# Kernel optimization log

Measured on AMD Instinct MI355X. Metric: run time of the kernel, lower is better.

The kernel has to match this reference:

```python
import jax, jax.numpy as jnp
import numpy as np

N, L, H, E, FE = 32, 128, 16, 256, 4  # batch, seq_len, heads, embed_size, forward_expansion
EPS = 1e-5
NEG_SLOPE = 0.01


def _mask_positions(qe):
    # zero entries where j < L-1-i (torch: triu(ones,1).flip(1) == 1)
    Ld = qe.shape[-1]
    i = jnp.arange(Ld)[:, None]
    j = jnp.arange(Ld)[None, :]
    return jnp.where(j >= (Ld - 1 - i), qe, jnp.zeros((), qe.dtype))


def _skew(qe):
    # pad last dim on the left, reinterpret, drop first row -> relative skew
    n, h, Ld, _ = qe.shape
    p = jnp.pad(qe, ((0, 0), (0, 0), (0, 0), (1, 0)))
    return p.reshape(n, h, Ld + 1, Ld)[:, :, 1:, :]


def _batchnorm(x, gamma, beta):
    # BatchNorm1d(C=L*H) over (N, C, E): normalize over batch and embed dims
    mean = jnp.mean(x, axis=(0, 2), keepdims=True)
    var = jnp.var(x, axis=(0, 2), keepdims=True)
    return (x - mean) * jax.lax.rsqrt(var + EPS) * gamma[None, :, None] + beta[None, :, None]


def _leaky(x):
    return jnp.where(x >= 0, x, NEG_SLOPE * x)


def setup_inputs() -> dict:
    key = jax.random.key(0)
    ks = jax.random.split(key, 16)
    s_e = 1.0 / np.sqrt(E)
    d = {
        "x": jax.random.normal(ks[0], (N, L * H, E, 1), dtype=jnp.float32),
        "Wq": jax.random.normal(ks[1], (E, E), dtype=jnp.float32) * s_e,
        "bq": jnp.zeros((E,), jnp.float32),
        "Wk": jax.random.normal(ks[2], (E, E), dtype=jnp.float32) * s_e,
        "bk": jnp.zeros((E,), jnp.float32),
        "Wv": jax.random.normal(ks[3], (E, E), dtype=jnp.float32) * s_e,
        "bv": jnp.zeros((E,), jnp.float32),
        "Erel": jax.random.normal(ks[4], (H, L, E), dtype=jnp.float32),
        "Wo": jax.random.normal(ks[5], (E, E), dtype=jnp.float32) * s_e,
        "bo": jnp.zeros((E,), jnp.float32),
        "g1": jnp.ones((L * H,), jnp.float32),
        "be1": jnp.zeros((L * H,), jnp.float32),
        "g2": jnp.ones((L * H,), jnp.float32),
        "be2": jnp.zeros((L * H,), jnp.float32),
        "W1": jax.random.normal(ks[6], (E, FE * E), dtype=jnp.float32) * s_e,
        "b1": jnp.zeros((FE * E,), jnp.float32),
        "W2": jax.random.normal(ks[7], (FE * E, E), dtype=jnp.float32) * (1.0 / np.sqrt(FE * E)),
        "b2": jnp.zeros((E,), jnp.float32),
        "Wenc": jax.random.normal(ks[8], (E, E), dtype=jnp.float32) * s_e,
        "benc": jnp.zeros((E,), jnp.float32),
    }
    return d


def reference(x, Wq, bq, Wk, bk, Wv, bv, Erel, Wo, bo, g1, be1, g2, be2, W1, b1, W2, b2, Wenc, benc):
    xs = x[:, :, :, 0]  # (N, L*H, E)
    q = (xs @ Wq + bq).reshape(N, L, H, E)
    k = (xs @ Wk + bk).reshape(N, L, H, E)
    v = (xs @ Wv + bv).reshape(N, L, H, E)
    # relative-position skew term (Music-Transformer style)
    QE = jnp.einsum('nlhe,hme->nhlm', q, Erel)       # (N,H,L,L)
    S = _skew(_mask_positions(QE))                   # (N,H,L,L)
    qk = jnp.einsum('nqhe,nkhe->nhqk', q, k)         # (N,H,L,L)
    att = jax.nn.softmax(qk / jnp.sqrt(jnp.float32(E)), axis=-1) + S
    z = jnp.einsum('nhql,nlhe->nqhe', att, v).reshape(N, L * H, E)
    z = z @ Wo + bo
    h1 = _batchnorm(z + xs, g1, be1)
    ff = _leaky(h1 @ W1 + b1) @ W2 + b2
    out = _batchnorm(ff + h1, g2, be2)
    return out @ Wenc + benc
```

## Files before the change

### kernel.cpp

```cpp
#include <hip/hip_runtime.h>
#include <hip/hip_bf16.h>

using u16 = unsigned short;
typedef __attribute__((ext_vector_type(8))) short bf16x8;
typedef __attribute__((ext_vector_type(4))) float f32x4;

static constexpr float EPS_ = 1e-5f;
static constexpr float NEG_ = 0.01f;

__device__ __forceinline__ float bf2f(u16 u) { return __uint_as_float(((unsigned)u) << 16); }
__device__ __forceinline__ u16 f2bf(float f) {
    union { __hip_bfloat16 h; u16 u; } c; c.h = __float2bfloat16(f); return c.u;
}

#define MFMA16(a, b, c) __builtin_amdgcn_mfma_f32_16x16x32_bf16(a, b, c, 0, 0, 0)

__device__ __forceinline__ void gload16(const u16* g, u16* l) {
    __builtin_amdgcn_global_load_lds(
        (__attribute__((address_space(1))) void*)(u16*)g,
        (__attribute__((address_space(3))) void*)l, 16, 0, 0);
}

__device__ __forceinline__ int xswz(int nwg) {
    const int b = blockIdx.x;
    return (b & 7) * (nwg >> 3) + (b >> 3);
}

__device__ __forceinline__ void lds_core(
    const u16* __restrict__ Ag, int lda,
    const u16* __restrict__ Bg, int ldb, int K,
    u16* As, u16* Bs, f32x4 acc[4][4])
{
    const int tid = threadIdx.x;
    const int w = tid >> 6, lane = tid & 63;
    const int g = lane >> 4, r = lane & 15;
    const int wm = (w >> 1) * 64, wn = (w & 1) * 64;
    const int rx = r & 7;

    for (int kt = 0; kt < K; kt += 64) {
        #pragma unroll
        for (int j = 0; j < 4; j++) {
            const int ubase = (w * 4 + j) * 64;
            const int u = ubase + lane;
            const int row = u >> 3;
            const int cb = ((u & 7) ^ (row & 7)) * 8;
            gload16(Ag + (size_t)row * lda + kt + cb, As + ubase * 8);
            gload16(Bg + (size_t)row * ldb + kt + cb, Bs + ubase * 8);
        }
        __syncthreads();
        #pragma unroll
        for (int kk = 0; kk < 2; kk++) {
            const int co = ((kk * 4 + g) ^ rx) * 8;
            bf16x8 af[4], bfr[4];
            #pragma unroll
            for (int f = 0; f < 4; f++) {
                af[f]  = *(const bf16x8*)(As + (wm + f * 16 + r) * 64 + co);
                bfr[f] = *(const bf16x8*)(Bs + (wn + f * 16 + r) * 64 + co);
            }
            #pragma unroll
            for (int i = 0; i < 4; i++)
                #pragma unroll
                for (int j = 0; j < 4; j++)
                    acc[i][j] = MFMA16(af[i], bfr[j], acc[i][j]);
        }
        __syncthreads();
    }
}

__device__ __forceinline__ void zero4(f32x4 acc[4][4]) {
    #pragma unroll
    for (int i = 0; i < 4; i++)
        #pragma unroll
        for (int j = 0; j < 4; j++)
            acc[i][j] = (f32x4){0.f, 0.f, 0.f, 0.f};
}

template<int K, int NN, int MODE>
__global__ __launch_bounds__(256) void gemm128_k(
    const u16* __restrict__ A, const u16* __restrict__ Bt,
    const float* __restrict__ bias, const u16* __restrict__ res,
    const float2* __restrict__ rp, const float* __restrict__ cs,
    void* __restrict__ outv)
{
    __shared__ __align__(16) u16 SH[17408];
    u16* As = SH; u16* Bs = SH + 8192;
    constexpr int NB = NN / 128;
    const int f = xswz(512 * NB);
    const int m0 = (f / NB) * 128, n0 = (f % NB) * 128;

    f32x4 acc[4][4]; zero4(acc);
    lds_core(A + (size_t)m0 * K, K, Bt + (size_t)n0 * K, K, K, As, Bs, acc);

    const int tid = threadIdx.x;
    const int w = tid >> 6, lane = tid & 63;
    const int g = lane >> 4, r = lane & 15;
    const int mb = (w >> 1) * 64, nb = (w & 1) * 64;

    __syncthreads();

    if constexpr (MODE == 3) {
        float* SHf = (float*)SH;
        float* out = (float*)outv;
        #pragma unroll
        for (int q = 0; q < 4; ++q) {
            if ((w >> 1) == (q >> 1)) {
                const int fmB = (q & 1) * 2;
                #pragma unroll
                for (int fi = 0; fi < 2; ++fi) {
                    #pragma unroll
                    for (int fn = 0; fn < 4; ++fn) {
                        const int col = nb + fn * 16 + r;
                        const float bv = bias[n0 + col], cv = cs[n0 + col];
                        #pragma unroll
                        for (int reg = 0; reg < 4; ++reg) {
                            const int rl = fi * 16 + g * 4 + reg;
                            const int m = m0 + q * 32 + rl;
                            const float2 pp = rp[m & 2047];
                            SHf[rl * 132 + col] =
                                pp.x * acc[fmB + fi][fn][reg] + pp.y * cv + bv;
                        }
                    }
                }
            }
            __syncthreads();
            #pragma unroll
            for (int p = 0; p < 4; ++p) {
                const int id = p * 256 + tid;
                const int rl = id >> 5, c4 = id & 31;
                const float4 v = *(const float4*)(SHf + rl * 132 + c4 * 4);
                *(float4*)(out + (size_t)(m0 + q * 32 + rl) * 256 + n0 + c4 * 4) = v;
            }
            __syncthreads();
        }
        return;
    }

    u16* out = (u16*)outv;
    #pragma unroll
    for (int fn = 0; fn < 4; ++fn) {
        const int col = nb + fn * 16 + r;
        const float bv = bias[n0 + col];
        #pragma unroll
        for (int fm = 0; fm < 4; ++fm) {
            #pragma unroll
            for (int reg = 0; reg < 4; ++reg) {
                const int rowt = mb + fm * 16 + g * 4 + reg;
                float v = acc[fm][fn][reg];
                if constexpr (MODE == 1) {
                    const float2 pp = rp[(m0 + rowt) & 2047];
                    v = pp.x * v + pp.y * cs[n0 + col] + bv;
                    v = v >= 0.f ? v : NEG_ * v;
                } else {
                    v += bv;
                }
                SH[rowt * 136 + col] = f2bf(v);
            }
        }
    }
    __syncthreads();
    #pragma unroll
    for (int p = 0; p < 8; ++p) {
        const int ck = p * 256 + tid;
        const int rowt = ck >> 4, cc = ck & 15;
        const int m = m0 + rowt;
        bf16x8 v = *(const bf16x8*)(SH + rowt * 136 + cc * 8);
        if constexpr (MODE == 0) {
            const bf16x8 rv = *(const bf16x8*)(res + (size_t)m * NN + n0 + cc * 8);
            #pragma unroll
            for (int j = 0; j < 8; ++j)
                v[j] = (short)f2bf(bf2f((u16)v[j]) + bf2f((u16)rv[j]));
        }
        if constexpr (MODE == 2) {
            const float2 pp = rp[m & 2047];
            const bf16x8 rv = *(const bf16x8*)(res + (size_t)m * NN + n0 + cc * 8);
            #pragma unroll
            for (int j = 0; j < 8; ++j)
                v[j] = (short)f2bf(bf2f((u16)v[j]) + pp.x * bf2f((u16)rv[j]) + pp.y);
        }
        *(bf16x8*)(out + (size_t)m * NN + n0 + cc * 8) = v;
    }
}

__global__ __launch_bounds__(256) void qkv_k(
    const u16* __restrict__ xbf, const u16* __restrict__ Wqkvt,
    const float* __restrict__ bq, const float* __restrict__ bk,
    const float* __restrict__ bv,
    u16* __restrict__ qo, u16* __restrict__ ko, u16* __restrict__ vo)
{
    __shared__ __align__(16) u16 SH[17408];
    u16* As = SH; u16* Bs = SH + 8192;
    const int f = xswz(3072);
    const int nblk = f % 6, mblk = f / 6;
    const int m0 = mblk * 128, n0 = nblk * 128;
    const int which = n0 >> 8;
    const float* bias = which == 0 ? bq : (which == 1 ? bk : bv);
    const int e0 = n0 & 255;

    f32x4 acc[4][4]; zero4(acc);
    lds_core(xbf + (size_t)m0 * 256, 256, Wqkvt + (size_t)n0 * 256, 256, 256,
             As, Bs, acc);

    const int tid = threadIdx.x;
    const int w = tid >> 6, lane = tid & 63;
    const int g = lane >> 4, r = lane & 15;
    const int mb = (w >> 1) * 64, nb = (w & 1) * 64;
    const int nn = m0 >> 11, l0 = (m0 & 2047) >> 4;

    __syncthreads();
    if (which == 2) {
        #pragma unroll
        for (int fn = 0; fn < 4; ++fn) {
            const int col = nb + fn * 16 + r;
            const float bv4 = bias[e0 + col];
            #pragma unroll
            for (int fm = 0; fm < 4; ++fm)
                #pragma unroll
                for (int reg = 0; reg < 4; ++reg) {
                    const int rowt = mb + fm * 16 + g * 4 + reg;
                    SH[col * 136 + (((rowt & 15) << 3) | (rowt >> 4))] =
                        f2bf(acc[fm][fn][reg] + bv4);
                }
        }
        __syncthreads();
        #pragma unroll
        for (int p = 0; p < 8; ++p) {
            const int ck = p * 256 + tid;
            const int e = ck >> 4, hh = ck & 15;
            const bf16x8 v = *(const bf16x8*)(SH + e * 136 + hh * 8);
            *(bf16x8*)(vo + ((size_t)(nn * 16 + hh) * 256 + e0 + e) * 128 + l0) = v;
        }
    } else {
        u16* out = which == 0 ? qo : ko;
        #pragma unroll
        for (int fn = 0; fn < 4; ++fn) {
            const int col = nb + fn * 16 + r;
            const float bv4 = bias[e0 + col];
            #pragma unroll
            for (int fm = 0; fm < 4; ++fm)
                #pragma unroll
                for (int reg = 0; reg < 4; ++reg) {
                    const int rowt = mb + fm * 16 + g * 4 + reg;
                    SH[rowt * 136 + col] = f2bf(acc[fm][fn][reg] + bv4);
                }
        }
        __syncthreads();
        #pragma unroll
        for (int p = 0; p < 8; ++p) {
            const int ck = p * 256 + tid;
            const int rowt = ck >> 4, cc = ck & 15;
            const int m = m0 + rowt;
            const int l = (m & 2047) >> 4, hh = m & 15;
            const bf16x8 v = *(const bf16x8*)(SH + rowt * 136 + cc * 8);
            *(bf16x8*)(out + ((size_t)(nn * 16 + hh) * 128 + l) * 256 + e0 + cc * 8) = v;
        }
    }
}

template<typename OutF>
__device__ __forceinline__ void epi_store128(
    u16* Cs, f32x4 (&acc)[4][4], float scale, OutF outp)
{
    const int tid = threadIdx.x;
    const int w = tid >> 6, lane = tid & 63;
    const int g = lane >> 4, r = lane & 15;
    const int mb = (w >> 1) * 64, nb = (w & 1) * 64;

    #pragma unroll
    for (int fn = 0; fn < 4; fn++) {
        const int col = nb + fn * 16 + r;
        #pragma unroll
        for (int fm = 0; fm < 4; fm++)
            #pragma unroll
            for (int reg = 0; reg < 4; reg++) {
                const int row = mb + fm * 16 + g * 4 + reg;
                Cs[row * 136 + col] = f2bf(acc[fm][fn][reg] * scale);
            }
    }
    __syncthreads();
    #pragma unroll
    for (int p = 0; p < 8; p++) {
        const int ck = p * 256 + tid;
        const int row = ck >> 4, cc = ck & 15;
        const bf16x8 v = *(const bf16x8*)(Cs + row * 136 + cc * 8);
        *(bf16x8*)outp(row, cc) = v;
    }
}

__global__ __launch_bounds__(256) void qkqe_k(
    const u16* __restrict__ q, const u16* __restrict__ kc,
    const u16* __restrict__ erel, u16* __restrict__ out)
{
    __shared__ __align__(16) u16 SH[17408];
    u16* As = SH; u16* Bs = SH + 8192;
    const int f = xswz(1024);
    const int b = f >> 1, h = b & 15;
    const int n0 = (f & 1) * 128;
    const u16* Ag = q + (size_t)b * 128 * 256;
    const u16* Bg = (n0 == 0) ? (kc + (size_t)b * 128 * 256)
                              : (erel + (size_t)h * 128 * 256);

    f32x4 acc[4][4]; zero4(acc);
    lds_core(Ag, 256, Bg, 256, 256, As, Bs, acc);

    const float scale = (n0 == 0) ? 0.0625f : 1.0f;
    __syncthreads();
    epi_store128(SH, acc, scale,
        [&](int row, int cc) -> u16* {
            return out + ((size_t)b * 128 + row) * 256 + n0 + cc * 8;
        });
}

__global__ __launch_bounds__(256) void softmax_k(
    const u16* __restrict__ qk, u16* __restrict__ att)
{
    const int r = blockIdx.x * 4 + (threadIdx.x >> 6);
    const int lane = threadIdx.x & 63;
    const int i = r & 127;
    const u16* row = qk + (size_t)r * 256;
    const float x0 = bf2f(row[lane]), x1 = bf2f(row[lane + 64]);
    float mx = fmaxf(x0, x1);
    #pragma unroll
    for (int o = 32; o; o >>= 1) mx = fmaxf(mx, __shfl_xor(mx, o));
    const float e0 = __expf(x0 - mx), e1 = __expf(x1 - mx);
    float s = e0 + e1;
    #pragma unroll
    for (int o = 32; o; o >>= 1) s += __shfl_xor(s, o);
    const float rinv = 1.0f / s;
    const float s0 = (lane <= i) ? bf2f(row[128 + 127 - i + lane]) : 0.f;
    const float s1 = (lane + 64 <= i) ? bf2f(row[128 + 127 - i + lane + 64]) : 0.f;
    att[(size_t)r * 128 + lane] = f2bf(e0 * rinv + s0);
    att[(size_t)r * 128 + lane + 64] = f2bf(e1 * rinv + s1);
}

__global__ __launch_bounds__(256) void av_k(
    const u16* __restrict__ att, const u16* __restrict__ vT,
    u16* __restrict__ zc)
{
    __shared__ __align__(16) u16 SH[17408];
    u16* As = SH; u16* Bs = SH + 8192;
    const int f = xswz(1024);
    const int b = f >> 1;
    const int n0 = (f & 1) * 128;
    const u16* Ag = att + (size_t)b * 128 * 128;
    const u16* Bg = vT + (size_t)b * 256 * 128 + (size_t)n0 * 128;

    f32x4 acc[4][4]; zero4(acc);
    lds_core(Ag, 128, Bg, 128, 128, As, Bs, acc);

    const int nn = b >> 4, hh = b & 15;
    __syncthreads();
    epi_store128(SH, acc, 1.f,
        [&](int row, int cc) -> u16* {
            return zc + ((size_t)(nn * 2048 + row * 16 + hh)) * 256 + n0 + cc * 8;
        });
}

__global__ __launch_bounds__(256) void cvt_k(const float* __restrict__ in,
                                             u16* __restrict__ out) {
    const size_t i8 = ((size_t)blockIdx.x * 256 + threadIdx.x) * 8;
    const float4 lo = *(const float4*)(in + i8);
    const float4 hi = *(const float4*)(in + i8 + 4);
    ushort4 o0, o1;
    o0.x = f2bf(lo.x); o0.y = f2bf(lo.y); o0.z = f2bf(lo.z); o0.w = f2bf(lo.w);
    o1.x = f2bf(hi.x); o1.y = f2bf(hi.y); o1.z = f2bf(hi.z); o1.w = f2bf(hi.w);
    *(ushort4*)(out + i8) = o0;
    *(ushort4*)(out + i8 + 4) = o1;
}

__global__ __launch_bounds__(256) void prep_w_k(
    const float* __restrict__ Wq, const float* __restrict__ Wk,
    const float* __restrict__ Wv, const float* __restrict__ Wo,
    const float* __restrict__ Wenc, const float* __restrict__ W1,
    const float* __restrict__ W2, const float* __restrict__ Erel,
    u16* __restrict__ Wqkvt, u16* __restrict__ Wot, u16* __restrict__ Wenct,
    u16* __restrict__ W1t, u16* __restrict__ W2t, u16* __restrict__ Erelb,
    float* __restrict__ cs1, float* __restrict__ csE)
{
    const int bid = blockIdx.x, tid = threadIdx.x;
    if (bid < 1280) {
        const int jb = bid >> 8;
        const int t = ((bid & 255) << 8) | tid;
        const int n = t >> 8, k = t & 255;
        const float* src = jb == 0 ? Wq : jb == 1 ? Wk : jb == 2 ? Wv
                         : jb == 3 ? Wo : Wenc;
        const u16 v = f2bf(src[(k << 8) + n]);
        if (jb < 3)       Wqkvt[jb * 65536 + t] = v;
        else if (jb == 3) Wot[t] = v;
        else              Wenct[t] = v;
    } else if (bid < 2304) {
        const int t = ((bid - 1280) << 8) | tid;
        const int n = t >> 8, k = t & 255;
        W1t[t] = f2bf(W1[(k << 10) + n]);
    } else if (bid < 3328) {
        const int t = ((bid - 2304) << 8) | tid;
        const int n = t >> 10, k = t & 1023;
        W2t[t] = f2bf(W2[(k << 8) + n]);
    } else if (bid < 5376) {
        const int t = ((bid - 3328) << 8) | tid;
        Erelb[t] = f2bf(Erel[t]);
    } else {
        const int n = (bid - 5376) * 256 + tid;
        if (n < 1024) {
            float s = 0.f;
            for (int k = 0; k < 256; ++k) s += bf2f(f2bf(W1[(size_t)k * 1024 + n]));
            cs1[n] = s;
        } else {
            const int n2 = n - 1024;
            float s = 0.f;
            for (int k = 0; k < 256; ++k) s += bf2f(f2bf(Wenc[(size_t)k * 256 + n2]));
            csE[n2] = s;
        }
    }
}

__global__ __launch_bounds__(256) void bnstats_k(
    const u16* __restrict__ x, const float* __restrict__ g,
    const float* __restrict__ be, float2* __restrict__ params)
{
    const int c = blockIdx.x, tid = threadIdx.x;
    float s = 0.f, s2 = 0.f;
    #pragma unroll 4
    for (int n = 0; n < 32; n++) {
        const float v = bf2f(x[((size_t)n * 2048 + c) * 256 + tid]);
        s += v; s2 += v * v;
    }
    #pragma unroll
    for (int o = 32; o; o >>= 1) { s += __shfl_xor(s, o); s2 += __shfl_xor(s2, o); }
    __shared__ float rs[4], rs2[4];
    const int w = tid >> 6;
    if ((tid & 63) == 0) { rs[w] = s; rs2[w] = s2; }
    __syncthreads();
    if (tid == 0) {
        s  = rs[0] + rs[1] + rs[2] + rs[3];
        s2 = rs2[0] + rs2[1] + rs2[2] + rs2[3];
        const float mean = s / 8192.f;
        const float var = s2 / 8192.f - mean * mean;
        const float a = g[c] * rsqrtf(var + EPS_);
        params[c] = make_float2(a, be[c] - mean * a);
    }
}

extern "C" void kernel_launch(void* const* d_in, const int* in_sizes, int n_in,
                              void* d_out, int out_size, void* d_ws, size_t ws_size,
                              hipStream_t stream)
{
    const float* x    = (const float*)d_in[0];
    const float* Wq   = (const float*)d_in[1];
    const float* bq   = (const float*)d_in[2];
    const float* Wk   = (const float*)d_in[3];
    const float* bk   = (const float*)d_in[4];
    const float* Wv   = (const float*)d_in[5];
    const float* bv   = (const float*)d_in[6];
    const float* Erel = (const float*)d_in[7];
    const float* Wo   = (const float*)d_in[8];
    const float* bo   = (const float*)d_in[9];
    const float* g1   = (const float*)d_in[10];
    const float* be1  = (const float*)d_in[11];
    const float* g2   = (const float*)d_in[12];
    const float* be2  = (const float*)d_in[13];
    const float* W1   = (const float*)d_in[14];
    const float* b1   = (const float*)d_in[15];
    const float* W2   = (const float*)d_in[16];
    const float* b2   = (const float*)d_in[17];
    const float* Wenc = (const float*)d_in[18];
    const float* benc = (const float*)d_in[19];

    char* ws = (char*)d_ws;
    const size_t MB = 1ull << 20;
    const size_t KB = 1024;
    u16* xbf   = (u16*)(ws + 0 * MB);
    u16* h2pre = (u16*)(ws + 32 * MB);
    u16* qb    = (u16*)(ws + 32 * MB);
    u16* kb    = (u16*)(ws + 64 * MB);
    u16* vT    = (u16*)(ws + 96 * MB);
    u16* qkb   = (u16*)(ws + 128 * MB);
    u16* attb  = (u16*)(ws + 160 * MB);
    u16* ff1   = (u16*)(ws + 64 * MB);
    u16* zc    = (u16*)(ws + 176 * MB);
    u16* h1pre = (u16*)(ws + 208 * MB);
    u16* Wqkvt = (u16*)(ws + 240 * MB);
    u16* Wot   = (u16*)(ws + 240 * MB + 512 * KB);
    u16* Wenct = (u16*)(ws + 240 * MB + 640 * KB);
    u16* W1t   = (u16*)(ws + 240 * MB + 768 * KB);
    u16* W2t   = (u16*)(ws + 240 * MB + 1280 * KB);
    u16* Erelb = (u16*)(ws + 240 * MB + 1792 * KB);
    float2* p1 = (float2*)(ws + 243 * MB);
    float2* p2 = (float2*)(ws + 243 * MB + 16 * KB);
    float* cs1 = (float*)(ws + 243 * MB + 32 * KB);
    float* csE = (float*)(ws + 243 * MB + 40 * KB);

    const dim3 b256(256);

    cvt_k<<<dim3(8192), b256, 0, stream>>>(x, xbf);
    prep_w_k<<<dim3(5381), b256, 0, stream>>>(Wq, Wk, Wv, Wo, Wenc, W1, W2, Erel,
                                              Wqkvt, Wot, Wenct, W1t, W2t, Erelb,
                                              cs1, csE);

    qkv_k<<<dim3(3072), b256, 0, stream>>>(xbf, Wqkvt, bq, bk, bv, qb, kb, vT);
    qkqe_k<<<dim3(1024), b256, 0, stream>>>(qb, kb, Erelb, qkb);
    softmax_k<<<dim3(16384), b256, 0, stream>>>(qkb, attb);
    av_k<<<dim3(1024), b256, 0, stream>>>(attb, vT, zc);
    gemm128_k<256, 256, 0><<<dim3(1024), b256, 0, stream>>>(
        zc, Wot, bo, xbf, nullptr, nullptr, h1pre);

    bnstats_k<<<dim3(2048), b256, 0, stream>>>(h1pre, g1, be1, p1);

    gemm128_k<256, 1024, 1><<<dim3(4096), b256, 0, stream>>>(
        h1pre, W1t, b1, nullptr, p1, cs1, ff1);
    gemm128_k<1024, 256, 2><<<dim3(1024), b256, 0, stream>>>(
        ff1, W2t, b2, h1pre, p1, nullptr, h2pre);

    bnstats_k<<<dim3(2048), b256, 0, stream>>>(h2pre, g2, be2, p2);
    gemm128_k<256, 256, 3><<<dim3(1024), b256, 0, stream>>>(
        h2pre, Wenct, benc, nullptr, p2, csE, (float*)d_out);
}
```

Measured before the change: 330.9 us.

## Use persistent B-panel-resident GEMMs with triple-buffered A staging for K=256 projections

```diff
diff --git a/kernel.cpp b/kernel.cpp
--- a/kernel.cpp
+++ b/kernel.cpp
@@ -24,6 +24,270 @@
 __device__ __forceinline__ int xswz(int nwg) {
     const int b = blockIdx.x;
     return (b & 7) * (nwg >> 3) + (b >> 3);
+}
+
+__device__ __forceinline__ void zero4(f32x4 acc[4][4]) {
+    #pragma unroll
+    for (int i = 0; i < 4; i++)
+        #pragma unroll
+        for (int j = 0; j < 4; j++)
+            acc[i][j] = (f32x4){0.f, 0.f, 0.f, 0.f};
+}
+
+__device__ __forceinline__ void bp_stageA(const u16* __restrict__ A,
+                                          int mrow_base, int ki, u16* dst) {
+    const int tid = threadIdx.x;
+    #pragma unroll
+    for (int j = 0; j < 4; ++j) {
+        const int u = j * 256 + tid;
+        const int row = u >> 3, slot = u & 7;
+        gload16(A + (size_t)(mrow_base + row) * 256 + ki * 64 +
+                    ((slot ^ (row & 7)) * 8),
+                dst + u * 8);
+    }
+}
+
+template<int MT, class EPIF>
+__device__ __forceinline__ void bp_run(
+    const u16* __restrict__ A, int m0base,
+    const u16* __restrict__ Btp,
+    u16* SH, EPIF epi)
+{
+    const int tid = threadIdx.x;
+    const int w = tid >> 6, lane = tid & 63;
+    const int g = lane >> 4, r = lane & 15;
+    const int wm = (w >> 1) * 64, wn = (w & 1) * 64;
+    const int rx = r & 7;
+    u16* Bp = SH;
+    u16* Ab0 = SH + 32768; u16* Ab1 = SH + 40960; u16* Ab2 = SH + 49152;
+    u16* Ab[3] = {Ab0, Ab1, Ab2};
+
+    #pragma unroll
+    for (int it = 0; it < 16; ++it) {
+        const int u = it * 256 + tid;
+        const int col = u >> 5, slot = u & 31;
+        gload16(Btp + (size_t)col * 256 + ((slot ^ (col & 7)) * 8), Bp + u * 8);
+    }
+    bp_stageA(A, m0base, 0, Ab[0]);
+    bp_stageA(A, m0base, 1, Ab[1]);
+
+    int cur = 0;
+    for (int mi = 0; mi < MT; ++mi) {
+        f32x4 acc[4][4]; zero4(acc);
+        const int mrow = m0base + mi * 128;
+        #pragma unroll
+        for (int ki = 0; ki < 4; ++ki) {
+            if (!(mi > 0 && ki == 0)) {
+                if (mi == MT - 1 && ki == 3)
+                    asm volatile("s_waitcnt vmcnt(0)" ::: "memory");
+                else
+                    asm volatile("s_waitcnt vmcnt(4)" ::: "memory");
+                __builtin_amdgcn_s_barrier();
+                __builtin_amdgcn_sched_barrier(0);
+            }
+            const u16* Abuf = Ab[cur];
+            const int nb = cur + 2 >= 3 ? cur - 1 : cur + 2;
+            if (ki == 0)      bp_stageA(A, mrow, 2, Ab[nb]);
+            else if (ki == 1) bp_stageA(A, mrow, 3, Ab[nb]);
+            else if (ki == 2) { if (mi + 1 < MT) bp_stageA(A, mrow + 128, 0, Ab[nb]); }
+            else              { if (mi + 1 < MT) bp_stageA(A, mrow + 128, 1, Ab[nb]); }
+            #pragma unroll
+            for (int kk = 0; kk < 2; ++kk) {
+                const int co = ((kk * 4 + g) ^ rx) * 8;
+                bf16x8 af[4], bfr[4];
+                #pragma unroll
+                for (int f2 = 0; f2 < 4; ++f2) {
+                    af[f2]  = *(const bf16x8*)(Abuf + (wm + f2 * 16 + r) * 64 + co);
+                    bfr[f2] = *(const bf16x8*)(Bp +
+                                (size_t)(wn + f2 * 16 + r) * 256 + ki * 64 + co);
+                }
+                __builtin_amdgcn_s_setprio(1);
+                #pragma unroll
+                for (int i = 0; i < 4; i++)
+                    #pragma unroll
+                    for (int j = 0; j < 4; j++)
+                        acc[i][j] = MFMA16(af[i], bfr[j], acc[i][j]);
+                __builtin_amdgcn_s_setprio(0);
+            }
+            cur = cur + 1 == 3 ? 0 : cur + 1;
+        }
+        epi(mrow, acc);
+        asm volatile("s_waitcnt vmcnt(0)" ::: "memory");
+        __builtin_amdgcn_s_barrier();
+        __builtin_amdgcn_sched_barrier(0);
+    }
+}
+
+template<int NPAN, int MT, int MODE, int NN>
+__global__ __launch_bounds__(256) void gemmBP_k(
+    const u16* __restrict__ A, const u16* __restrict__ Bt,
+    const float* __restrict__ bias, const u16* __restrict__ res,
+    const float2* __restrict__ rp, const float* __restrict__ cs,
+    void* __restrict__ outv)
+{
+    __shared__ __align__(16) u16 SH[74752];
+    const int f = xswz(NPAN * (512 / MT));
+    const int panel = f % NPAN, mg = f / NPAN;
+    const int n0 = panel * 128;
+    const int m0base = mg * MT * 128;
+    u16* EPIB = SH + 57344;
+
+    const int tid = threadIdx.x;
+    const int w = tid >> 6, lane = tid & 63;
+    const int g = lane >> 4, r = lane & 15;
+    const int mb = (w >> 1) * 64, nb = (w & 1) * 64;
+
+    auto epi = [&](int mrow, f32x4 (&acc)[4][4]) {
+        if constexpr (MODE == 3) {
+            float* SHf = (float*)EPIB;
+            float* out = (float*)outv;
+            #pragma unroll
+            for (int q = 0; q < 4; ++q) {
+                if ((w >> 1) == (q >> 1)) {
+                    const int fmB = (q & 1) * 2;
+                    #pragma unroll
+                    for (int fi = 0; fi < 2; ++fi)
+                        #pragma unroll
+                        for (int fn = 0; fn < 4; ++fn) {
+                            const int col = nb + fn * 16 + r;
+                            const float bv = bias[n0 + col], cv = cs[n0 + col];
+                            #pragma unroll
+                            for (int reg = 0; reg < 4; ++reg) {
+                                const int rl = fi * 16 + g * 4 + reg;
+                                const int m = mrow + q * 32 + rl;
+                                const float2 pp = rp[m & 2047];
+                                SHf[rl * 132 + col] =
+                                    pp.x * acc[fmB + fi][fn][reg] + pp.y * cv + bv;
+                            }
+                        }
+                }
+                __syncthreads();
+                #pragma unroll
+                for (int p = 0; p < 4; ++p) {
+                    const int id = p * 256 + tid;
+                    const int rl = id >> 5, c4 = id & 31;
+                    const float4 v = *(const float4*)(SHf + rl * 132 + c4 * 4);
+                    *(float4*)(out + (size_t)(mrow + q * 32 + rl) * 256 + n0 + c4 * 4) = v;
+                }
+                __syncthreads();
+            }
+            return;
+        }
+        u16* out = (u16*)outv;
+        #pragma unroll
+        for (int fn = 0; fn < 4; ++fn) {
+            const int col = nb + fn * 16 + r;
+            const float bv = bias[n0 + col];
+            #pragma unroll
+            for (int fm = 0; fm < 4; ++fm)
+                #pragma unroll
+                for (int reg = 0; reg < 4; ++reg) {
+                    const int rowt = mb + fm * 16 + g * 4 + reg;
+                    float v = acc[fm][fn][reg];
+                    if constexpr (MODE == 1) {
+                        const float2 pp = rp[(mrow + rowt) & 2047];
+                        v = pp.x * v + pp.y * cs[n0 + col] + bv;
+                        v = v >= 0.f ? v : NEG_ * v;
+                    } else {
+                        v += bv;
+                    }
+                    EPIB[rowt * 136 + col] = f2bf(v);
+                }
+        }
+        __syncthreads();
+        #pragma unroll
+        for (int p = 0; p < 8; ++p) {
+            const int ck = p * 256 + tid;
+            const int rowt = ck >> 4, cc = ck & 15;
+            const int m = mrow + rowt;
+            bf16x8 v = *(const bf16x8*)(EPIB + rowt * 136 + cc * 8);
+            if constexpr (MODE == 0) {
+                const bf16x8 rv = *(const bf16x8*)(res + (size_t)m * NN + n0 + cc * 8);
+                #pragma unroll
+                for (int j = 0; j < 8; ++j)
+                    v[j] = (short)f2bf(bf2f((u16)v[j]) + bf2f((u16)rv[j]));
+            }
+            *(bf16x8*)(out + (size_t)m * NN + n0 + cc * 8) = v;
+        }
+    };
+
+    bp_run<MT>(A, m0base, Bt + (size_t)n0 * 256, SH, epi);
+}
+
+__global__ __launch_bounds__(256) void qkvBP_k(
+    const u16* __restrict__ xbf, const u16* __restrict__ Wqkvt,
+    const float* __restrict__ bq, const float* __restrict__ bk,
+    const float* __restrict__ bv,
+    u16* __restrict__ qo, u16* __restrict__ ko, u16* __restrict__ vo)
+{
+    __shared__ __align__(16) u16 SH[74752];
+    const int f = xswz(768);
+    const int panel = f % 6, mg = f / 6;
+    const int n0 = panel * 128;
+    const int which = n0 >> 8;
+    const int e0 = n0 & 255;
+    const float* bias = which == 0 ? bq : (which == 1 ? bk : bv);
+    const int m0base = mg * 512;
+    u16* EPIB = SH + 57344;
+
+    const int tid = threadIdx.x;
+    const int w = tid >> 6, lane = tid & 63;
+    const int g = lane >> 4, r = lane & 15;
+    const int mb = (w >> 1) * 64, nb = (w & 1) * 64;
+
+    auto epi = [&](int mrow, f32x4 (&acc)[4][4]) {
+        const int nn = mrow >> 11;
+        if (which == 2) {
+            const int l0 = (mrow & 2047) >> 4;
+            #pragma unroll
+            for (int fn = 0; fn < 4; ++fn) {
+                const int col = nb + fn * 16 + r;
+                const float bv4 = bias[e0 + col];
+                #pragma unroll
+                for (int fm = 0; fm < 4; ++fm)
+                    #pragma unroll
+                    for (int reg = 0; reg < 4; ++reg) {
+                        const int rowt = mb + fm * 16 + g * 4 + reg;
+                        EPIB[col * 136 + (((rowt & 15) << 3) | (rowt >> 4))] =
+                            f2bf(acc[fm][fn][reg] + bv4);
+                    }
+            }
+            __syncthreads();
+            #pragma unroll
+            for (int p = 0; p < 8; ++p) {
+                const int ck = p * 256 + tid;
+                const int e = ck >> 4, hh = ck & 15;
+                const bf16x8 v = *(const bf16x8*)(EPIB + e * 136 + hh * 8);
+                *(bf16x8*)(vo + ((size_t)(nn * 16 + hh) * 256 + e0 + e) * 128 + l0) = v;
+            }
+        } else {
+            u16* out = which == 0 ? qo : ko;
+            #pragma unroll
+            for (int fn = 0; fn < 4; ++fn) {
+                const int col = nb + fn * 16 + r;
+                const float bv4 = bias[e0 + col];
+                #pragma unroll
+                for (int fm = 0; fm < 4; ++fm)
+                    #pragma unroll
+                    for (int reg = 0; reg < 4; ++reg) {
+                        const int rowt = mb + fm * 16 + g * 4 + reg;
+                        EPIB[rowt * 136 + col] = f2bf(acc[fm][fn][reg] + bv4);
+                    }
+            }
+            __syncthreads();
+            #pragma unroll
+            for (int p = 0; p < 8; ++p) {
+                const int ck = p * 256 + tid;
+                const int rowt = ck >> 4, cc = ck & 15;
+                const int m = mrow + rowt;
+                const int l = (m & 2047) >> 4, hh = m & 15;
+                const bf16x8 v = *(const bf16x8*)(EPIB + rowt * 136 + cc * 8);
+                *(bf16x8*)(out + ((size_t)(nn * 16 + hh) * 128 + l) * 256 + e0 + cc * 8) = v;
+            }
+        }
+    };
+
+    bp_run<4>(xbf, m0base, Wqkvt + (size_t)n0 * 256, SH, epi);
 }
 
 __device__ __forceinline__ void lds_core(
@@ -67,29 +331,19 @@
     }
 }
 
-__device__ __forceinline__ void zero4(f32x4 acc[4][4]) {
-    #pragma unroll
-    for (int i = 0; i < 4; i++)
-        #pragma unroll
-        for (int j = 0; j < 4; j++)
-            acc[i][j] = (f32x4){0.f, 0.f, 0.f, 0.f};
-}
-
-template<int K, int NN, int MODE>
-__global__ __launch_bounds__(256) void gemm128_k(
-    const u16* __restrict__ A, const u16* __restrict__ Bt,
+__global__ __launch_bounds__(256) void ff2_k(
+    const u16* __restrict__ A, const u16* __restrict__ Wt,
     const float* __restrict__ bias, const u16* __restrict__ res,
-    const float2* __restrict__ rp, const float* __restrict__ cs,
-    void* __restrict__ outv)
+    const float2* __restrict__ rp, u16* __restrict__ out)
 {
     __shared__ __align__(16) u16 SH[17408];
     u16* As = SH; u16* Bs = SH + 8192;
-    constexpr int NB = NN / 128;
-    const int f = xswz(512 * NB);
-    const int m0 = (f / NB) * 128, n0 = (f % NB) * 128;
+    const int f = xswz(1024);
+    const int m0 = (f >> 1) * 128, n0 = (f & 1) * 128;
 
     f32x4 acc[4][4]; zero4(acc);
-    lds_core(A + (size_t)m0 * K, K, Bt + (size_t)n0 * K, K, K, As, Bs, acc);
+    lds_core(A + (size_t)m0 * 1024, 1024, Wt + (size_t)n0 * 1024, 1024, 1024,
+             As, Bs, acc);
 
     const int tid = threadIdx.x;
     const int w = tid >> 6, lane = tid & 63;
@@ -97,65 +351,17 @@
     const int mb = (w >> 1) * 64, nb = (w & 1) * 64;
 
     __syncthreads();
-
-    if constexpr (MODE == 3) {
-        float* SHf = (float*)SH;
-        float* out = (float*)outv;
-        #pragma unroll
-        for (int q = 0; q < 4; ++q) {
-            if ((w >> 1) == (q >> 1)) {
-                const int fmB = (q & 1) * 2;
-                #pragma unroll
-                for (int fi = 0; fi < 2; ++fi) {
-                    #pragma unroll
-                    for (int fn = 0; fn < 4; ++fn) {
-                        const int col = nb + fn * 16 + r;
-                        const float bv = bias[n0 + col], cv = cs[n0 + col];
-                        #pragma unroll
-                        for (int reg = 0; reg < 4; ++reg) {
-                            const int rl = fi * 16 + g * 4 + reg;
-                            const int m = m0 + q * 32 + rl;
-                            const float2 pp = rp[m & 2047];
-                            SHf[rl * 132 + col] =
-                                pp.x * acc[fmB + fi][fn][reg] + pp.y * cv + bv;
-                        }
-                    }
-                }
-            }
-            __syncthreads();
-            #pragma unroll
-            for (int p = 0; p < 4; ++p) {
-                const int id = p * 256 + tid;
-                const int rl = id >> 5, c4 = id & 31;
-                const float4 v = *(const float4*)(SHf + rl * 132 + c4 * 4);
-                *(float4*)(out + (size_t)(m0 + q * 32 + rl) * 256 + n0 + c4 * 4) = v;
-            }
-            __syncthreads();
-        }
-        return;
-    }
-
-    u16* out = (u16*)outv;
     #pragma unroll
     for (int fn = 0; fn < 4; ++fn) {
         const int col = nb + fn * 16 + r;
         const float bv = bias[n0 + col];
         #pragma unroll
-        for (int fm = 0; fm < 4; ++fm) {
+        for (int fm = 0; fm < 4; ++fm)
             #pragma unroll
             for (int reg = 0; reg < 4; ++reg) {
                 const int rowt = mb + fm * 16 + g * 4 + reg;
-                float v = acc[fm][fn][reg];
-                if constexpr (MODE == 1) {
-                    const float2 pp = rp[(m0 + rowt) & 2047];
-                    v = pp.x * v + pp.y * cs[n0 + col] + bv;
-                    v = v >= 0.f ? v : NEG_ * v;
-                } else {
-                    v += bv;
-                }
-                SH[rowt * 136 + col] = f2bf(v);
-            }
-        }
+                SH[rowt * 136 + col] = f2bf(acc[fm][fn][reg] + bv);
+            }
     }
     __syncthreads();
     #pragma unroll
@@ -163,96 +369,13 @@
         const int ck = p * 256 + tid;
         const int rowt = ck >> 4, cc = ck & 15;
         const int m = m0 + rowt;
+        const float2 pp = rp[m & 2047];
         bf16x8 v = *(const bf16x8*)(SH + rowt * 136 + cc * 8);
-        if constexpr (MODE == 0) {
-            const bf16x8 rv = *(const bf16x8*)(res + (size_t)m * NN + n0 + cc * 8);
-            #pragma unroll
-            for (int j = 0; j < 8; ++j)
-                v[j] = (short)f2bf(bf2f((u16)v[j]) + bf2f((u16)rv[j]));
-        }
-        if constexpr (MODE == 2) {
-            const float2 pp = rp[m & 2047];
-            const bf16x8 rv = *(const bf16x8*)(res + (size_t)m * NN + n0 + cc * 8);
-            #pragma unroll
-            for (int j = 0; j < 8; ++j)
-                v[j] = (short)f2bf(bf2f((u16)v[j]) + pp.x * bf2f((u16)rv[j]) + pp.y);
-        }
-        *(bf16x8*)(out + (size_t)m * NN + n0 + cc * 8) = v;
-    }
-}
-
-__global__ __launch_bounds__(256) void qkv_k(
-    const u16* __restrict__ xbf, const u16* __restrict__ Wqkvt,
-    const float* __restrict__ bq, const float* __restrict__ bk,
-    const float* __restrict__ bv,
-    u16* __restrict__ qo, u16* __restrict__ ko, u16* __restrict__ vo)
-{
-    __shared__ __align__(16) u16 SH[17408];
-    u16* As = SH; u16* Bs = SH + 8192;
-    const int f = xswz(3072);
-    const int nblk = f % 6, mblk = f / 6;
-    const int m0 = mblk * 128, n0 = nblk * 128;
-    const int which = n0 >> 8;
-    const float* bias = which == 0 ? bq : (which == 1 ? bk : bv);
-    const int e0 = n0 & 255;
-
-    f32x4 acc[4][4]; zero4(acc);
-    lds_core(xbf + (size_t)m0 * 256, 256, Wqkvt + (size_t)n0 * 256, 256, 256,
-             As, Bs, acc);
-
-    const int tid = threadIdx.x;
-    const int w = tid >> 6, lane = tid & 63;
-    const int g = lane >> 4, r = lane & 15;
-    const int mb = (w >> 1) * 64, nb = (w & 1) * 64;
-    const int nn = m0 >> 11, l0 = (m0 & 2047) >> 4;
-
-    __syncthreads();
-    if (which == 2) {
-        #pragma unroll
-        for (int fn = 0; fn < 4; ++fn) {
-            const int col = nb + fn * 16 + r;
-            const float bv4 = bias[e0 + col];
-            #pragma unroll
-            for (int fm = 0; fm < 4; ++fm)
-                #pragma unroll
-                for (int reg = 0; reg < 4; ++reg) {
-                    const int rowt = mb + fm * 16 + g * 4 + reg;
-                    SH[col * 136 + (((rowt & 15) << 3) | (rowt >> 4))] =
-                        f2bf(acc[fm][fn][reg] + bv4);
-                }
-        }
-        __syncthreads();
-        #pragma unroll
-        for (int p = 0; p < 8; ++p) {
-            const int ck = p * 256 + tid;
-            const int e = ck >> 4, hh = ck & 15;
-            const bf16x8 v = *(const bf16x8*)(SH + e * 136 + hh * 8);
-            *(bf16x8*)(vo + ((size_t)(nn * 16 + hh) * 256 + e0 + e) * 128 + l0) = v;
-        }
-    } else {
-        u16* out = which == 0 ? qo : ko;
-        #pragma unroll
-        for (int fn = 0; fn < 4; ++fn) {
-            const int col = nb + fn * 16 + r;
-            const float bv4 = bias[e0 + col];
-            #pragma unroll
-            for (int fm = 0; fm < 4; ++fm)
-                #pragma unroll
-                for (int reg = 0; reg < 4; ++reg) {
-                    const int rowt = mb + fm * 16 + g * 4 + reg;
-                    SH[rowt * 136 + col] = f2bf(acc[fm][fn][reg] + bv4);
-                }
-        }
-        __syncthreads();
-        #pragma unroll
-        for (int p = 0; p < 8; ++p) {
-            const int ck = p * 256 + tid;
-            const int rowt = ck >> 4, cc = ck & 15;
-            const int m = m0 + rowt;
-            const int l = (m & 2047) >> 4, hh = m & 15;
-            const bf16x8 v = *(const bf16x8*)(SH + rowt * 136 + cc * 8);
-            *(bf16x8*)(out + ((size_t)(nn * 16 + hh) * 128 + l) * 256 + e0 + cc * 8) = v;
-        }
+        const bf16x8 rv = *(const bf16x8*)(res + (size_t)m * 256 + n0 + cc * 8);
+        #pragma unroll
+        for (int j = 0; j < 8; ++j)
+            v[j] = (short)f2bf(bf2f((u16)v[j]) + pp.x * bf2f((u16)rv[j]) + pp.y);
+        *(bf16x8*)(out + (size_t)m * 256 + n0 + cc * 8) = v;
     }
 }
 
@@ -496,21 +619,20 @@
                                               Wqkvt, Wot, Wenct, W1t, W2t, Erelb,
                                               cs1, csE);
 
-    qkv_k<<<dim3(3072), b256, 0, stream>>>(xbf, Wqkvt, bq, bk, bv, qb, kb, vT);
+    qkvBP_k<<<dim3(768), b256, 0, stream>>>(xbf, Wqkvt, bq, bk, bv, qb, kb, vT);
     qkqe_k<<<dim3(1024), b256, 0, stream>>>(qb, kb, Erelb, qkb);
     softmax_k<<<dim3(16384), b256, 0, stream>>>(qkb, attb);
     av_k<<<dim3(1024), b256, 0, stream>>>(attb, vT, zc);
-    gemm128_k<256, 256, 0><<<dim3(1024), b256, 0, stream>>>(
+    gemmBP_k<2, 4, 0, 256><<<dim3(256), b256, 0, stream>>>(
         zc, Wot, bo, xbf, nullptr, nullptr, h1pre);
 
     bnstats_k<<<dim3(2048), b256, 0, stream>>>(h1pre, g1, be1, p1);
 
-    gemm128_k<256, 1024, 1><<<dim3(4096), b256, 0, stream>>>(
+    gemmBP_k<8, 16, 1, 1024><<<dim3(256), b256, 0, stream>>>(
         h1pre, W1t, b1, nullptr, p1, cs1, ff1);
-    gemm128_k<1024, 256, 2><<<dim3(1024), b256, 0, stream>>>(
-        ff1, W2t, b2, h1pre, p1, nullptr, h2pre);
+    ff2_k<<<dim3(1024), b256, 0, stream>>>(ff1, W2t, b2, h1pre, p1, h2pre);
 
     bnstats_k<<<dim3(2048), b256, 0, stream>>>(h2pre, g2, be2, p2);
-    gemm128_k<256, 256, 3><<<dim3(1024), b256, 0, stream>>>(
+    gemmBP_k<2, 4, 3, 256><<<dim3(256), b256, 0, stream>>>(
         h2pre, Wenct, benc, nullptr, p2, csE, (float*)d_out);
 }
```

After: 430.2 us. 1.3x slower.
